# Kernel tuning notes

Measured on AMD Instinct MI355X. Metric: run time of the kernel, lower is better.

## Reference

```python
import jax, jax.numpy as jnp
import numpy as np

B, L, C, Q, H = 32, 2048, 512, 512, 1024

def setup_inputs() -> dict:
    key = jax.random.key(0)
    ks = jax.random.split(key, 8)
    query = jax.random.normal(ks[0], (B, Q), dtype=jnp.float32)
    context = jax.random.normal(ks[1], (B, L, C), dtype=jnp.float32)
    mapping_mask = jax.random.randint(ks[2], (B, L, 1), 0, 2).astype(jnp.float32)
    s = 0.02
    Wq = jax.random.normal(ks[3], (H, Q), dtype=jnp.float32) * s
    Wc = jax.random.normal(ks[4], (H, C), dtype=jnp.float32) * s
    bc = jnp.zeros((H,), dtype=jnp.float32)
    Wo = jax.random.normal(ks[5], (1, H), dtype=jnp.float32) * s
    bo = jnp.zeros((1,), dtype=jnp.float32)
    return {"query": query, "context": context, "mapping_mask": mapping_mask,
            "Wq": Wq, "Wc": Wc, "bc": bc, "Wo": Wo, "bo": bo}

def reference(query, context, mapping_mask, Wq, Wc, bc, Wo, bo):
    # res_q: [B,H], res_c: [B,L,H]
    res_q = query @ Wq.T
    res_c = jnp.einsum('blc,hc->blh', context, Wc) + bc
    tmp = jnp.tanh(res_q[:, None, :] + res_c)            # [B,L,H]
    weights_logit = jnp.einsum('blh,oh->blo', tmp, Wo) + bo  # [B,L,1]
    weights_exp = mapping_mask * jnp.exp(weights_logit)      # unnormalized, no max-subtract (faithful)
    weights = weights_exp / (weights_exp.sum(axis=1, keepdims=True) + 1e-5)
    output = jnp.einsum('blo,blc->boc', weights, context)[:, 0, :]  # bmm(w^T, ctx) -> squeeze
    return output, weights
```

## Files before the change

kernel.cpp:

```cpp
#include <hip/hip_runtime.h>

#define NB 32
#define LL 2048
#define CH 512
#define BQ 512
#define HH 1024

typedef __attribute__((ext_vector_type(8))) short bf16x8;
typedef __attribute__((ext_vector_type(16))) float f32x16;

__device__ __forceinline__ unsigned int cvt_pk_bf16(float a, float b) {
  unsigned int r;
  asm("v_cvt_pk_bf16_f32 %0, %1, %2" : "=v"(r) : "v"(a), "v"(b));
  return r;
}

__device__ __forceinline__ float fast_tanh(float x) {
  float e = __builtin_amdgcn_exp2f(x * 2.885390081777927f);
  return 1.0f - 2.0f * __builtin_amdgcn_rcpf(e + 1.0f);
}

__global__ __launch_bounds__(256) void k_prep(const float* __restrict__ Wc,
                                              uint4* __restrict__ wcbp,
                                              const float* __restrict__ query,
                                              const float* __restrict__ Wq,
                                              const float* __restrict__ bc,
                                              float* __restrict__ resqc,
                                              float* __restrict__ logit,
                                              float* __restrict__ out) {
  int bid = blockIdx.x, t = threadIdx.x;
  if (bid < 256) {
    int gid = bid * 256 + t;
    int lane = gid & 63, ks = (gid >> 6) & 31, cg = gid >> 11;
    int lo = lane & 31, hi = lane >> 5;
    const float4* s = (const float4*)(Wc + (size_t)(cg * 32 + lo) * CH + hi * 8 + ks * 16);
    float4 v0 = s[0], v1 = s[1];
    uint4 p;
    p.x = cvt_pk_bf16(v0.x, v0.y);
    p.y = cvt_pk_bf16(v0.z, v0.w);
    p.z = cvt_pk_bf16(v1.x, v1.y);
    p.w = cvt_pk_bf16(v1.z, v1.w);
    wcbp[gid] = p;
  } else if (bid < 384) {
    int gid = (bid - 256) * 256 + t;
    int b = gid >> 10, h = gid & 1023;
    const float4* q4 = (const float4*)(query + (size_t)b * BQ);
    const float4* w4 = (const float4*)(Wq + (size_t)h * BQ);
    float acc = 0.f;
#pragma unroll 4
    for (int i = 0; i < BQ / 4; ++i) {
      float4 a = q4[i], w = w4[i];
      acc += a.x * w.x + a.y * w.y + a.z * w.z + a.w * w.w;
    }
    resqc[gid] = acc + bc[h];
  } else if (bid < 400) {
    float4* p = (float4*)logit + (bid - 384) * 1024 + t;
#pragma unroll
    for (int i = 0; i < 4; ++i) p[i * 256] = (float4){0, 0, 0, 0};
  } else {
    float4* p = (float4*)out + t;
#pragma unroll
    for (int i = 0; i < 16; ++i) p[i * 256] = (float4){0, 0, 0, 0};
  }
}

__global__ __launch_bounds__(512, 4) void k_logits_f(const float* __restrict__ ctx,
                                                     const uint4* __restrict__ bpk,
                                                     const float* __restrict__ resqc,
                                                     const float* __restrict__ Wo,
                                                     float* __restrict__ logit) {
  __shared__ unsigned short A[64 * 520];

  const int t = threadIdx.x;
  const int bid = blockIdx.x;
  const int swz = (bid & 7) * 256 + (bid >> 3);
  const int lt = swz >> 1, nh = swz & 1;
  const int b = lt >> 5, row0 = (lt & 31) << 6;

  const float4* src = (const float4*)(ctx + ((size_t)(b * LL + row0)) * CH);
#pragma unroll
  for (int i = 0; i < 16; ++i) {
    int f = i * 512 + t;
    int r = f >> 7, c4 = f & 127;
    float4 v = src[f];
    uint2 w;
    w.x = cvt_pk_bf16(v.x, v.y);
    w.y = cvt_pk_bf16(v.z, v.w);
    *(uint2*)(A + r * 520 + c4 * 4) = w;
  }
  __syncthreads();

  const int wv = t >> 6, lane = t & 63;
  const int lo = lane & 31, hi = lane >> 5;

  const int wvu = __builtin_amdgcn_readfirstlane(wv);
  const char* b0 = (const char*)(bpk + (size_t)((nh * 16 + wvu * 2) * 32) * 64);
  const char* b1 = b0 + 32768;
  const unsigned vo = lane * 16;

  const char* a0 = (const char*)A + lo * 1040 + hi * 16;

  f32x16 acc[2][2];
#pragma unroll
  for (int m = 0; m < 2; ++m)
#pragma unroll
    for (int n = 0; n < 2; ++n) acc[m][n] = (f32x16){0,0,0,0,0,0,0,0,0,0,0,0,0,0,0,0};

  for (int kg = 0; kg < 8; ++kg) {
#pragma unroll
    for (int j = 0; j < 4; ++j) {
      uint4 ub0 = *(const uint4*)(b0 + vo + j * 1024);
      uint4 ub1 = *(const uint4*)(b1 + vo + j * 1024);
      bf16x8 fa0 = *(const bf16x8*)(a0 + kg * 128 + j * 32);
      bf16x8 fa1 = *(const bf16x8*)(a0 + 33280 + kg * 128 + j * 32);
      bf16x8 fb0, fb1;
      __builtin_memcpy(&fb0, &ub0, 16);
      __builtin_memcpy(&fb1, &ub1, 16);
      acc[0][0] = __builtin_amdgcn_mfma_f32_32x32x16_bf16(fa0, fb0, acc[0][0], 0, 0, 0);
      acc[0][1] = __builtin_amdgcn_mfma_f32_32x32x16_bf16(fa0, fb1, acc[0][1], 0, 0, 0);
      acc[1][0] = __builtin_amdgcn_mfma_f32_32x32x16_bf16(fa1, fb0, acc[1][0], 0, 0, 0);
      acc[1][1] = __builtin_amdgcn_mfma_f32_32x32x16_bf16(fa1, fb1, acc[1][1], 0, 0, 0);
    }
    b0 += 4096; b1 += 4096;
  }

  const int c0 = nh * 512 + wv * 64;
  float q0 = resqc[b * HH + c0 + lo], q1 = resqc[b * HH + c0 + 32 + lo];
  float w0 = Wo[c0 + lo],             w1 = Wo[c0 + 32 + lo];
  float v[32];
#pragma unroll
  for (int m = 0; m < 2; ++m)
#pragma unroll
    for (int r = 0; r < 16; ++r)
      v[m * 16 + r] = w0 * fast_tanh(acc[m][0][r] + q0)
                    + w1 * fast_tanh(acc[m][1][r] + q1);
#pragma unroll
  for (int sdist = 16; sdist >= 1; sdist >>= 1) {
#pragma unroll
    for (int i = 0; i < sdist; ++i) {
      float a = v[i], c = v[i + sdist];
      float keep = (lo & sdist) ? c : a;
      float send = (lo & sdist) ? a : c;
      v[i] = keep + __shfl_xor(send, sdist, 64);
    }
  }
  int rr = lo & 15;
  int row_local = (lo >> 4) * 32 + (rr & 3) + 8 * (rr >> 2) + 4 * hi;
  atomicAdd(&logit[(size_t)b * LL + row0 + row_local], v[0]);
}

__global__ __launch_bounds__(256) void k_weights(const float* __restrict__ mask,
                                                 const float* __restrict__ bo,
                                                 const float* __restrict__ logit,
                                                 float* __restrict__ wout) {
  __shared__ float red[4];
  int b = blockIdx.x, t = threadIdx.x;
  float bov = bo[0];
  float w[8];
  float s = 0.f;
#pragma unroll
  for (int i = 0; i < 8; ++i) {
    int l = t + 256 * i;
    float e = mask[b * LL + l] * __expf(logit[b * LL + l] + bov);
    w[i] = e; s += e;
  }
#pragma unroll
  for (int m = 32; m >= 1; m >>= 1) s += __shfl_xor(s, m, 64);
  int wave = t >> 6, lane = t & 63;
  if (lane == 0) red[wave] = s;
  __syncthreads();
  float inv = 1.0f / (red[0] + red[1] + red[2] + red[3] + 1e-5f);
#pragma unroll
  for (int i = 0; i < 8; ++i) wout[b * LL + t + 256 * i] = w[i] * inv;
}

__global__ __launch_bounds__(256) void k_output_f32(const float* __restrict__ ctx,
                                                    const float* __restrict__ weights,
                                                    float* __restrict__ out) {
  __shared__ float wl[128];
  int bid = blockIdx.x;
  int b = bid >> 4, chunk = bid & 15;
  int t = threadIdx.x;
  int l0 = chunk * 128;
  if (t < 128) wl[t] = weights[b * LL + l0 + t];
  __syncthreads();
  const float2* c2 = (const float2*)(ctx + ((size_t)(b * LL + l0)) * CH) + t;
  float ax = 0.f, ay = 0.f;
#pragma unroll 4
  for (int l = 0; l < 128; ++l) {
    float wv = wl[l];
    float2 v = c2[(size_t)l * (CH / 2)];
    ax += wv * v.x; ay += wv * v.y;
  }
  atomicAdd(&out[b * CH + 2 * t], ax);
  atomicAdd(&out[b * CH + 2 * t + 1], ay);
}

extern "C" void kernel_launch(void* const* d_in, const int* in_sizes, int n_in,
                              void* d_out, int out_size, void* d_ws, size_t ws_size,
                              hipStream_t stream) {
  const float* query = (const float*)d_in[0];
  const float* ctx   = (const float*)d_in[1];
  const float* mask  = (const float*)d_in[2];
  const float* Wq    = (const float*)d_in[3];
  const float* Wc    = (const float*)d_in[4];
  const float* bc    = (const float*)d_in[5];
  const float* Wo    = (const float*)d_in[6];
  const float* bo    = (const float*)d_in[7];
  float* out = (float*)d_out;

  uint4* wcbp  = (uint4*)d_ws;
  float* resqc = (float*)((char*)d_ws + (1 << 20));
  float* logit = (float*)((char*)d_ws + (1 << 20) + (1 << 17));
  float* wout = out + NB * CH;

  k_prep<<<401, 256, 0, stream>>>(Wc, wcbp, query, Wq, bc, resqc, logit, out);
  k_logits_f<<<2048, 512, 0, stream>>>(ctx, wcbp, resqc, Wo, logit);
  k_weights<<<32, 256, 0, stream>>>(mask, bo, logit, wout);
  k_output_f32<<<512, 256, 0, stream>>>(ctx, wout, out);
}
```

Measured before the change: 125.6 us.

## Make logits kernel persistent with register-resident Wc slice and double-buffered context tiles

The logits kernel goes from 2048 blocks that each load one 64-row context tile and stream Wc from global memory to 512 blocks. Each block keeps a 32-column Wc slice resident in registers per wave and loops over 8 row tiles. The next context tile is prefetched and converted to bf16 into a second LDS buffer while MFMAs run on the current one. This cuts repeated Wc loads and overlaps context loading with compute. In exchange it raises register pressure (32 bf16x8 fragments per lane), halves occupancy, and issues 4x more context reads per Wc column group.

```diff
diff --git a/kernel.cpp b/kernel.cpp
--- a/kernel.cpp
+++ b/kernel.cpp
@@ -64,89 +64,127 @@
   }
 }
 
-__global__ __launch_bounds__(512, 4) void k_logits_f(const float* __restrict__ ctx,
+__global__ __launch_bounds__(512, 2) void k_logits_r(const float* __restrict__ ctx,
                                                      const uint4* __restrict__ bpk,
                                                      const float* __restrict__ resqc,
                                                      const float* __restrict__ Wo,
                                                      float* __restrict__ logit) {
-  __shared__ unsigned short A[64 * 520];
+  __shared__ unsigned short A[2][64 * 520];
 
   const int t = threadIdx.x;
   const int bid = blockIdx.x;
-  const int swz = (bid & 7) * 256 + (bid >> 3);
-  const int lt = swz >> 1, nh = swz & 1;
-  const int b = lt >> 5, row0 = (lt & 31) << 6;
-
-  const float4* src = (const float4*)(ctx + ((size_t)(b * LL + row0)) * CH);
-#pragma unroll
-  for (int i = 0; i < 16; ++i) {
-    int f = i * 512 + t;
-    int r = f >> 7, c4 = f & 127;
-    float4 v = src[f];
-    uint2 w;
-    w.x = cvt_pk_bf16(v.x, v.y);
-    w.y = cvt_pk_bf16(v.z, v.w);
-    *(uint2*)(A + r * 520 + c4 * 4) = w;
-  }
-  __syncthreads();
-
+  const int wid = (bid & 7) * 64 + (bid >> 3);
+  const int cg = wid & 3, rr = wid >> 2;
+  const int b = rr >> 2;
+  const int lbase = (rr & 3) * 512;
   const int wv = t >> 6, lane = t & 63;
   const int lo = lane & 31, hi = lane >> 5;
 
-  const int wvu = __builtin_amdgcn_readfirstlane(wv);
-  const char* b0 = (const char*)(bpk + (size_t)((nh * 16 + wvu * 2) * 32) * 64);
-  const char* b1 = b0 + 32768;
-  const unsigned vo = lane * 16;
-
-  const char* a0 = (const char*)A + lo * 1040 + hi * 16;
-
-  f32x16 acc[2][2];
-#pragma unroll
-  for (int m = 0; m < 2; ++m)
-#pragma unroll
-    for (int n = 0; n < 2; ++n) acc[m][n] = (f32x16){0,0,0,0,0,0,0,0,0,0,0,0,0,0,0,0};
-
-  for (int kg = 0; kg < 8; ++kg) {
-#pragma unroll
-    for (int j = 0; j < 4; ++j) {
-      uint4 ub0 = *(const uint4*)(b0 + vo + j * 1024);
-      uint4 ub1 = *(const uint4*)(b1 + vo + j * 1024);
-      bf16x8 fa0 = *(const bf16x8*)(a0 + kg * 128 + j * 32);
-      bf16x8 fa1 = *(const bf16x8*)(a0 + 33280 + kg * 128 + j * 32);
-      bf16x8 fb0, fb1;
-      __builtin_memcpy(&fb0, &ub0, 16);
-      __builtin_memcpy(&fb1, &ub1, 16);
-      acc[0][0] = __builtin_amdgcn_mfma_f32_32x32x16_bf16(fa0, fb0, acc[0][0], 0, 0, 0);
-      acc[0][1] = __builtin_amdgcn_mfma_f32_32x32x16_bf16(fa0, fb1, acc[0][1], 0, 0, 0);
-      acc[1][0] = __builtin_amdgcn_mfma_f32_32x32x16_bf16(fa1, fb0, acc[1][0], 0, 0, 0);
-      acc[1][1] = __builtin_amdgcn_mfma_f32_32x32x16_bf16(fa1, fb1, acc[1][1], 0, 0, 0);
-    }
-    b0 += 4096; b1 += 4096;
-  }
-
-  const int c0 = nh * 512 + wv * 64;
-  float q0 = resqc[b * HH + c0 + lo], q1 = resqc[b * HH + c0 + 32 + lo];
-  float w0 = Wo[c0 + lo],             w1 = Wo[c0 + 32 + lo];
-  float v[32];
-#pragma unroll
-  for (int m = 0; m < 2; ++m)
-#pragma unroll
-    for (int r = 0; r < 16; ++r)
-      v[m * 16 + r] = w0 * fast_tanh(acc[m][0][r] + q0)
-                    + w1 * fast_tanh(acc[m][1][r] + q1);
-#pragma unroll
-  for (int sdist = 16; sdist >= 1; sdist >>= 1) {
-#pragma unroll
-    for (int i = 0; i < sdist; ++i) {
-      float a = v[i], c = v[i + sdist];
-      float keep = (lo & sdist) ? c : a;
-      float send = (lo & sdist) ? a : c;
-      v[i] = keep + __shfl_xor(send, sdist, 64);
-    }
-  }
-  int rr = lo & 15;
-  int row_local = (lo >> 4) * 32 + (rr & 3) + 8 * (rr >> 2) + 4 * hi;
-  atomicAdd(&logit[(size_t)b * LL + row0 + row_local], v[0]);
+  const int cg32 = cg * 8 + wv;
+  bf16x8 fbreg[32];
+  {
+    const uint4* bp = bpk + (size_t)cg32 * 2048 + lane;
+#pragma unroll
+    for (int ks = 0; ks < 32; ++ks) {
+      uint4 u = bp[ks * 64];
+      __builtin_memcpy(&fbreg[ks], &u, 16);
+    }
+  }
+  const int c0 = cg32 * 32;
+  const float q0 = resqc[b * HH + c0 + lo];
+  const float w0 = Wo[c0 + lo];
+
+  const float* actx = ctx + ((size_t)(b * LL + lbase)) * CH;
+
+  {
+    const float4* src = (const float4*)actx;
+#pragma unroll
+    for (int i = 0; i < 16; ++i) {
+      int f = i * 512 + t;
+      int r = f >> 7, c4 = f & 127;
+      float4 v = src[f];
+      uint2 w;
+      w.x = cvt_pk_bf16(v.x, v.y);
+      w.y = cvt_pk_bf16(v.z, v.w);
+      *(uint2*)(A[0] + r * 520 + c4 * 4) = w;
+    }
+  }
+  __syncthreads();
+
+  for (int tt = 0; tt < 8; ++tt) {
+    const char* a0 = (const char*)(A[tt & 1]) + lo * 1040 + hi * 16;
+    unsigned short* An = A[(tt + 1) & 1];
+    const float4* srcn = (const float4*)(actx + (size_t)(tt + 1) * 64 * CH);
+
+    f32x16 acc0 = {0,0,0,0,0,0,0,0,0,0,0,0,0,0,0,0};
+    f32x16 acc1 = {0,0,0,0,0,0,0,0,0,0,0,0,0,0,0,0};
+
+    float4 sv[8];
+    if (tt < 7) {
+#pragma unroll
+      for (int i = 0; i < 8; ++i) sv[i] = srcn[i * 512 + t];
+    }
+#pragma unroll
+    for (int ks = 0; ks < 16; ++ks) {
+      bf16x8 fa0 = *(const bf16x8*)(a0 + ks * 32);
+      bf16x8 fa1 = *(const bf16x8*)(a0 + 33280 + ks * 32);
+      acc0 = __builtin_amdgcn_mfma_f32_32x32x16_bf16(fa0, fbreg[ks], acc0, 0, 0, 0);
+      acc1 = __builtin_amdgcn_mfma_f32_32x32x16_bf16(fa1, fbreg[ks], acc1, 0, 0, 0);
+    }
+    if (tt < 7) {
+#pragma unroll
+      for (int i = 0; i < 8; ++i) {
+        int f = i * 512 + t;
+        int r = f >> 7, c4 = f & 127;
+        uint2 w;
+        w.x = cvt_pk_bf16(sv[i].x, sv[i].y);
+        w.y = cvt_pk_bf16(sv[i].z, sv[i].w);
+        *(uint2*)(An + r * 520 + c4 * 4) = w;
+      }
+#pragma unroll
+      for (int i = 0; i < 8; ++i) sv[i] = srcn[(8 + i) * 512 + t];
+    }
+#pragma unroll
+    for (int ks = 16; ks < 32; ++ks) {
+      bf16x8 fa0 = *(const bf16x8*)(a0 + ks * 32);
+      bf16x8 fa1 = *(const bf16x8*)(a0 + 33280 + ks * 32);
+      acc0 = __builtin_amdgcn_mfma_f32_32x32x16_bf16(fa0, fbreg[ks], acc0, 0, 0, 0);
+      acc1 = __builtin_amdgcn_mfma_f32_32x32x16_bf16(fa1, fbreg[ks], acc1, 0, 0, 0);
+    }
+    if (tt < 7) {
+#pragma unroll
+      for (int i = 0; i < 8; ++i) {
+        int f = (8 + i) * 512 + t;
+        int r = f >> 7, c4 = f & 127;
+        uint2 w;
+        w.x = cvt_pk_bf16(sv[i].x, sv[i].y);
+        w.y = cvt_pk_bf16(sv[i].z, sv[i].w);
+        *(uint2*)(An + r * 520 + c4 * 4) = w;
+      }
+    }
+
+    float v[32];
+#pragma unroll
+    for (int r = 0; r < 16; ++r) {
+      v[r]      = w0 * fast_tanh(acc0[r] + q0);
+      v[16 + r] = w0 * fast_tanh(acc1[r] + q0);
+    }
+#pragma unroll
+    for (int sdist = 16; sdist >= 1; sdist >>= 1) {
+#pragma unroll
+      for (int i = 0; i < sdist; ++i) {
+        float a = v[i], c = v[i + sdist];
+        float keep = (lo & sdist) ? c : a;
+        float send = (lo & sdist) ? a : c;
+        v[i] = keep + __shfl_xor(send, sdist, 64);
+      }
+    }
+    int rm = lo & 15;
+    int row_local = (lo >> 4) * 32 + (rm & 3) + 8 * (rm >> 2) + 4 * hi;
+    atomicAdd(&logit[(size_t)b * LL + lbase + tt * 64 + row_local], v[0]);
+
+    __syncthreads();
+  }
 }
 
 __global__ __launch_bounds__(256) void k_weights(const float* __restrict__ mask,
@@ -215,7 +253,7 @@
   float* wout = out + NB * CH;
 
   k_prep<<<401, 256, 0, stream>>>(Wc, wcbp, query, Wq, bc, resqc, logit, out);
-  k_logits_f<<<2048, 512, 0, stream>>>(ctx, wcbp, resqc, Wo, logit);
+  k_logits_r<<<512, 512, 0, stream>>>(ctx, wcbp, resqc, Wo, logit);
   k_weights<<<32, 256, 0, stream>>>(mask, bo, logit, wout);
   k_output_f32<<<512, 256, 0, stream>>>(ctx, wout, out);
 }
```

New measurement: 130.8 us. 1.04x slower.

## Retile logits GEMM to 256x256 with double-buffered K pipeline and LDS-direct B loads

Applied to the files above, without the earlier changes.

Restructures the main logits GEMM from 64-row tiles (each needing the full K in LDS) to 256x256 output tiles that iterate over K in 64-wide steps. The A tile is converted fp32→bf16 into double-buffered swizzled LDS, and the B tile is loaded through global_load_lds. Loads for the next step overlap MFMA work, with explicit waitcnt, barriers and setprio. This cuts redundant reads of Wc and ctx per output and hides global latency, at the cost of using 128KB LDS, allowing only two blocks per CU, and more register pressure.

```diff
diff --git a/kernel.cpp b/kernel.cpp
--- a/kernel.cpp
+++ b/kernel.cpp
@@ -18,6 +18,11 @@
 __device__ __forceinline__ float fast_tanh(float x) {
   float e = __builtin_amdgcn_exp2f(x * 2.885390081777927f);
   return 1.0f - 2.0f * __builtin_amdgcn_rcpf(e + 1.0f);
+}
+
+__device__ __forceinline__ void glds16(const void* g, void* l) {
+  __builtin_amdgcn_global_load_lds((const __attribute__((address_space(1))) void*)g,
+                                   (__attribute__((address_space(3))) void*)l, 16, 0, 0);
 }
 
 __global__ __launch_bounds__(256) void k_prep(const float* __restrict__ Wc,
@@ -64,89 +69,159 @@
   }
 }
 
-__global__ __launch_bounds__(512, 4) void k_logits_f(const float* __restrict__ ctx,
+__global__ __launch_bounds__(512, 2) void k_logits_t(const float* __restrict__ ctx,
                                                      const uint4* __restrict__ bpk,
                                                      const float* __restrict__ resqc,
                                                      const float* __restrict__ Wo,
                                                      float* __restrict__ logit) {
-  __shared__ unsigned short A[64 * 520];
+  __shared__ char lds[131072];
 
   const int t = threadIdx.x;
   const int bid = blockIdx.x;
-  const int swz = (bid & 7) * 256 + (bid >> 3);
-  const int lt = swz >> 1, nh = swz & 1;
-  const int b = lt >> 5, row0 = (lt & 31) << 6;
-
-  const float4* src = (const float4*)(ctx + ((size_t)(b * LL + row0)) * CH);
-#pragma unroll
-  for (int i = 0; i < 16; ++i) {
-    int f = i * 512 + t;
-    int r = f >> 7, c4 = f & 127;
-    float4 v = src[f];
-    uint2 w;
-    w.x = cvt_pk_bf16(v.x, v.y);
-    w.y = cvt_pk_bf16(v.z, v.w);
-    *(uint2*)(A + r * 520 + c4 * 4) = w;
-  }
-  __syncthreads();
-
+  const int g = (bid & 7) * 128 + (bid >> 3);
+  const int mtile = g >> 2, ntile = g & 3;
   const int wv = t >> 6, lane = t & 63;
+  const int wm = wv >> 2, wn = wv & 3;
   const int lo = lane & 31, hi = lane >> 5;
-
-  const int wvu = __builtin_amdgcn_readfirstlane(wv);
-  const char* b0 = (const char*)(bpk + (size_t)((nh * 16 + wvu * 2) * 32) * 64);
-  const char* b1 = b0 + 32768;
-  const unsigned vo = lane * 16;
-
-  const char* a0 = (const char*)A + lo * 1040 + hi * 16;
-
-  f32x16 acc[2][2];
-#pragma unroll
-  for (int m = 0; m < 2; ++m)
+  const int b = mtile >> 3;
+
+  const int c0 = ntile * 256 + wn * 64;
+  const float q0 = resqc[b * HH + c0 + lo], q1 = resqc[b * HH + c0 + 32 + lo];
+  const float w0 = Wo[c0 + lo],             w1 = Wo[c0 + 32 + lo];
+
+  const float* actx = ctx + (size_t)mtile * 256 * CH;
+
+  int soff[4], sdst[4];
+#pragma unroll
+  for (int w = 0; w < 4; ++w) {
+    int f = w * 512 + t;
+    int row = f >> 3, c8 = f & 7;
+    soff[w] = row * CH + c8 * 8;
+    sdst[w] = ((row >> 5) * 8 + c8) * 512 + 16 * ((row & 31) ^ c8);
+  }
+  int aro[4];
+#pragma unroll
+  for (int ks = 0; ks < 4; ++ks) {
+    int c8 = ks * 2 + hi;
+    aro[ks] = c8 * 512 + 16 * (lo ^ c8);
+  }
+  const uint4* bsrc0 = bpk + ((size_t)(ntile * 8 + wv) * 32) * 64 + lane;
+
+  float4 av[8];
+
+#define LOADA(kt)                                                              \
+  {                                                                            \
+    _Pragma("unroll") for (int w = 0; w < 4; ++w) {                            \
+      const float4* s = (const float4*)(actx + (size_t)soff[w] + (kt) * 64);   \
+      av[2 * w] = s[0]; av[2 * w + 1] = s[1];                                  \
+    }                                                                          \
+  }
+#define WRITEA(p)                                                              \
+  {                                                                            \
+    _Pragma("unroll") for (int w = 0; w < 4; ++w) {                            \
+      uint4 pk;                                                                \
+      pk.x = cvt_pk_bf16(av[2 * w].x, av[2 * w].y);                            \
+      pk.y = cvt_pk_bf16(av[2 * w].z, av[2 * w].w);                            \
+      pk.z = cvt_pk_bf16(av[2 * w + 1].x, av[2 * w + 1].y);                    \
+      pk.w = cvt_pk_bf16(av[2 * w + 1].z, av[2 * w + 1].w);                    \
+      *(uint4*)(lds + (p) * 32768 + sdst[w]) = pk;                             \
+    }                                                                          \
+  }
+#define GLDSB(kt, p)                                                           \
+  {                                                                            \
+    _Pragma("unroll") for (int j = 0; j < 4; ++j)                              \
+      glds16(bsrc0 + ((size_t)(kt) * 4 + j) * 64,                              \
+             lds + 65536 + (p) * 32768 + (wv * 4 + j) * 1024);                 \
+  }
+#define COMPUTE(p, KS0, KS1)                                                   \
+  {                                                                            \
+    _Pragma("unroll") for (int ks = (KS0); ks <= (KS1); ++ks) {                \
+      bf16x8 fb0 = *(const bf16x8*)(lds + 65536 + (p) * 32768 +                \
+                                    ((wn * 2 + 0) * 4 + ks) * 1024 + lane * 16); \
+      bf16x8 fb1 = *(const bf16x8*)(lds + 65536 + (p) * 32768 +                \
+                                    ((wn * 2 + 1) * 4 + ks) * 1024 + lane * 16); \
+      _Pragma("unroll") for (int m = 0; m < 4; ++m) {                          \
+        bf16x8 fa = *(const bf16x8*)(lds + (p) * 32768 + (wm * 4 + m) * 4096 + \
+                                     aro[ks]);                                 \
+        acc[m][0] = __builtin_amdgcn_mfma_f32_32x32x16_bf16(fa, fb0, acc[m][0], 0, 0, 0); \
+        acc[m][1] = __builtin_amdgcn_mfma_f32_32x32x16_bf16(fa, fb1, acc[m][1], 0, 0, 0); \
+      }                                                                        \
+    }                                                                          \
+  }
+
+  f32x16 acc[4][2];
+#pragma unroll
+  for (int m = 0; m < 4; ++m)
 #pragma unroll
     for (int n = 0; n < 2; ++n) acc[m][n] = (f32x16){0,0,0,0,0,0,0,0,0,0,0,0,0,0,0,0};
 
-  for (int kg = 0; kg < 8; ++kg) {
-#pragma unroll
-    for (int j = 0; j < 4; ++j) {
-      uint4 ub0 = *(const uint4*)(b0 + vo + j * 1024);
-      uint4 ub1 = *(const uint4*)(b1 + vo + j * 1024);
-      bf16x8 fa0 = *(const bf16x8*)(a0 + kg * 128 + j * 32);
-      bf16x8 fa1 = *(const bf16x8*)(a0 + 33280 + kg * 128 + j * 32);
-      bf16x8 fb0, fb1;
-      __builtin_memcpy(&fb0, &ub0, 16);
-      __builtin_memcpy(&fb1, &ub1, 16);
-      acc[0][0] = __builtin_amdgcn_mfma_f32_32x32x16_bf16(fa0, fb0, acc[0][0], 0, 0, 0);
-      acc[0][1] = __builtin_amdgcn_mfma_f32_32x32x16_bf16(fa0, fb1, acc[0][1], 0, 0, 0);
-      acc[1][0] = __builtin_amdgcn_mfma_f32_32x32x16_bf16(fa1, fb0, acc[1][0], 0, 0, 0);
-      acc[1][1] = __builtin_amdgcn_mfma_f32_32x32x16_bf16(fa1, fb1, acc[1][1], 0, 0, 0);
+  LOADA(0);
+  GLDSB(0, 0);
+  WRITEA(0);
+  LOADA(1);
+  asm volatile("s_waitcnt vmcnt(8) lgkmcnt(0)" ::: "memory");
+  __builtin_amdgcn_sched_barrier(0);
+  __builtin_amdgcn_s_barrier();
+  __builtin_amdgcn_sched_barrier(0);
+
+#pragma unroll
+  for (int kt = 0; kt < 8; ++kt) {
+    const int p = kt & 1, pn = p ^ 1;
+    if (kt < 7) GLDSB(kt + 1, pn);
+    __builtin_amdgcn_sched_barrier(0);
+    __builtin_amdgcn_s_setprio(1);
+    COMPUTE(p, 0, 1);
+    __builtin_amdgcn_s_setprio(0);
+    __builtin_amdgcn_sched_barrier(0);
+    if (kt < 7) WRITEA(pn);
+    __builtin_amdgcn_sched_barrier(0);
+    if (kt < 6) LOADA(kt + 2);
+    __builtin_amdgcn_sched_barrier(0);
+    __builtin_amdgcn_s_setprio(1);
+    COMPUTE(p, 2, 3);
+    __builtin_amdgcn_s_setprio(0);
+    __builtin_amdgcn_sched_barrier(0);
+    if (kt < 6) {
+      asm volatile("s_waitcnt vmcnt(8) lgkmcnt(0)" ::: "memory");
+      __builtin_amdgcn_sched_barrier(0);
+      __builtin_amdgcn_s_barrier();
+      __builtin_amdgcn_sched_barrier(0);
+    } else if (kt == 6) {
+      asm volatile("s_waitcnt vmcnt(0) lgkmcnt(0)" ::: "memory");
+      __builtin_amdgcn_sched_barrier(0);
+      __builtin_amdgcn_s_barrier();
+      __builtin_amdgcn_sched_barrier(0);
     }
-    b0 += 4096; b1 += 4096;
-  }
-
-  const int c0 = nh * 512 + wv * 64;
-  float q0 = resqc[b * HH + c0 + lo], q1 = resqc[b * HH + c0 + 32 + lo];
-  float w0 = Wo[c0 + lo],             w1 = Wo[c0 + 32 + lo];
-  float v[32];
-#pragma unroll
-  for (int m = 0; m < 2; ++m)
-#pragma unroll
-    for (int r = 0; r < 16; ++r)
-      v[m * 16 + r] = w0 * fast_tanh(acc[m][0][r] + q0)
-                    + w1 * fast_tanh(acc[m][1][r] + q1);
-#pragma unroll
-  for (int sdist = 16; sdist >= 1; sdist >>= 1) {
-#pragma unroll
-    for (int i = 0; i < sdist; ++i) {
-      float a = v[i], c = v[i + sdist];
-      float keep = (lo & sdist) ? c : a;
-      float send = (lo & sdist) ? a : c;
-      v[i] = keep + __shfl_xor(send, sdist, 64);
+  }
+
+#pragma unroll
+  for (int rp = 0; rp < 2; ++rp) {
+    float v[32];
+#pragma unroll
+    for (int mm = 0; mm < 2; ++mm)
+#pragma unroll
+      for (int r = 0; r < 16; ++r)
+        v[mm * 16 + r] = w0 * fast_tanh(acc[rp * 2 + mm][0][r] + q0)
+                       + w1 * fast_tanh(acc[rp * 2 + mm][1][r] + q1);
+#pragma unroll
+    for (int sdist = 16; sdist >= 1; sdist >>= 1) {
+#pragma unroll
+      for (int i = 0; i < sdist; ++i) {
+        float a = v[i], c = v[i + sdist];
+        float keep = (lo & sdist) ? c : a;
+        float send = (lo & sdist) ? a : c;
+        v[i] = keep + __shfl_xor(send, sdist, 64);
+      }
     }
-  }
-  int rr = lo & 15;
-  int row_local = (lo >> 4) * 32 + (rr & 3) + 8 * (rr >> 2) + 4 * hi;
-  atomicAdd(&logit[(size_t)b * LL + row0 + row_local], v[0]);
+    int rr = lo & 15;
+    int m = rp * 2 + (lo >> 4);
+    int grow = mtile * 256 + wm * 128 + m * 32 + (rr & 3) + 8 * (rr >> 2) + 4 * hi;
+    atomicAdd(&logit[grow], v[0]);
+  }
+#undef LOADA
+#undef WRITEA
+#undef GLDSB
+#undef COMPUTE
 }
 
 __global__ __launch_bounds__(256) void k_weights(const float* __restrict__ mask,
@@ -215,7 +290,7 @@
   float* wout = out + NB * CH;
 
   k_prep<<<401, 256, 0, stream>>>(Wc, wcbp, query, Wq, bc, resqc, logit, out);
-  k_logits_f<<<2048, 512, 0, stream>>>(ctx, wcbp, resqc, Wo, logit);
+  k_logits_t<<<1024, 512, 0, stream>>>(ctx, wcbp, resqc, Wo, logit);
   k_weights<<<32, 256, 0, stream>>>(mask, bo, logit, wout);
   k_output_f32<<<512, 256, 0, stream>>>(ctx, wout, out);
 }
```

Result: slower. 130.5 us (+3.9%).
